# Optimization experiments

Measured on AMD Instinct MI355X. Metric: run time of the kernel, lower is better.

## Reference

```python
import jax, jax.numpy as jnp
import numpy as np

B, N, K = 2, 1280, 48
C_NODE, C_EDGE, C_OUT = 384, 128, 128
C_BIAS = C_NODE // 2          # 192 (node_dilation=2)
HID = 2 * C_BIAS + C_EDGE     # 512
LN_EPS = 1e-5


def setup_inputs() -> dict:
    key = jax.random.key(0)
    ks = jax.random.split(key, 13)
    w = lambda k, shape: (jax.random.normal(k, shape, jnp.float32) * 0.02)
    return {
        "node_emb": jax.random.normal(ks[0], (B, N, C_NODE), jnp.float32),
        "edge_emb": jax.random.normal(ks[1], (B, N, K, C_EDGE), jnp.float32),
        "E_idx": jax.random.randint(ks[2], (B, N, K), 0, N),
        "Wi": w(ks[3], (C_NODE, C_BIAS)), "bi": jnp.zeros((C_BIAS,), jnp.float32),
        "W1": w(ks[4], (HID, HID)), "b1": jnp.zeros((HID,), jnp.float32),
        "W2": w(ks[5], (HID, HID)), "b2": jnp.zeros((HID,), jnp.float32),
        "Wf": w(ks[6], (HID, C_OUT)), "bf": jnp.zeros((C_OUT,), jnp.float32),
        "gamma": jnp.ones((C_OUT,), jnp.float32),
        "beta": jnp.zeros((C_OUT,), jnp.float32),
    }


def reference(node_emb, edge_emb, E_idx, Wi, bi, W1, b1, W2, b2, Wf, bf, gamma, beta):
    # initial_embed: [B, N, C_NODE] -> [B, N, C_BIAS]
    n = node_emb @ Wi + bi
    # edge_bias[b,i,k] = concat(n[b,i], n[b, E_idx[b,i,k]])  (tile + gather_edges fused)
    nbr = jax.vmap(lambda v, e: v[e])(n, E_idx)                     # [B, N, K, C_BIAS]
    slf = jnp.broadcast_to(n[:, :, None, :], nbr.shape)             # [B, N, K, C_BIAS]
    x = jnp.concatenate([edge_emb, slf, nbr], axis=-1)              # [B, N, K, HID]
    h = jax.nn.relu(x @ W1 + b1)
    h = jax.nn.relu(h @ W2 + b2)
    # final_layer on residual sum, then LayerNorm
    y = (h + x) @ Wf + bf                                           # [B, N, K, C_OUT]
    mu = jnp.mean(y, axis=-1, keepdims=True)
    var = jnp.mean((y - mu) ** 2, axis=-1, keepdims=True)
    return (y - mu) * jax.lax.rsqrt(var + LN_EPS) * gamma + beta
```

## Files before the change

kernel.cpp:

```cpp
#include <hip/hip_runtime.h>
#include <stdint.h>

#define BB    2
#define NN    1280
#define KK    48
#define CN    384
#define CE    128
#define CB    192
#define HID   512
#define CO    128
#define MM    (BB*NN*KK)
#define CH    (MM/2)

typedef __bf16 bf16x8 __attribute__((ext_vector_type(8)));
typedef float  f32x4  __attribute__((ext_vector_type(4)));
typedef unsigned short u16x8 __attribute__((ext_vector_type(8)));

__device__ __forceinline__ unsigned short f2bf(float f) {
  unsigned int i = __builtin_bit_cast(unsigned int, f);
  unsigned int r = (i + 0x7fffu + ((i >> 16) & 1u)) >> 16;
  return (unsigned short)r;
}
__device__ __forceinline__ float bf2f(unsigned short u) {
  unsigned int v = ((unsigned int)u) << 16;
  return __builtin_bit_cast(float, v);
}

__device__ __forceinline__ void gload_lds16(const void* g, void* l) {
  __builtin_amdgcn_global_load_lds(
      (const __attribute__((address_space(1))) void*)g,
      (__attribute__((address_space(3))) void*)l, 16, 0, 0);
}

__device__ __forceinline__ void mfma_tiles(const char* ldsA, const char* ldsB,
                                           int l, int wm, int wn,
                                           f32x4 (&acc)[4][4]) {
#pragma unroll
  for (int kk = 0; kk < 2; ++kk) {
    bf16x8 av[4], bv[4];
#pragma unroll
    for (int t = 0; t < 4; ++t) {
      const int ra = wm * 64 + t * 16 + (l & 15);
      const int ca = (kk * 4 + (l >> 4)) ^ (ra & 7);
      av[t] = *(const bf16x8*)(ldsA + ra * 128 + ca * 16);
      const int rb = wn * 64 + t * 16 + (l & 15);
      const int cb = (kk * 4 + (l >> 4)) ^ (rb & 7);
      bv[t] = *(const bf16x8*)(ldsB + rb * 128 + cb * 16);
    }
#pragma unroll
    for (int mt = 0; mt < 4; ++mt)
#pragma unroll
      for (int nt = 0; nt < 4; ++nt)
        acc[mt][nt] = __builtin_amdgcn_mfma_f32_16x16x32_bf16(av[mt], bv[nt], acc[mt][nt], 0, 0, 0);
  }
}

__global__ void k_transpose_cast(const float* __restrict__ in,
                                 unsigned short* __restrict__ out,
                                 int R, int C) {
  __shared__ float tile[32][33];
  const int c0 = blockIdx.x * 32, r0 = blockIdx.y * 32;
  const int tx = threadIdx.x, ty = threadIdx.y;
#pragma unroll
  for (int dy = 0; dy < 32; dy += 8)
    tile[ty + dy][tx] = in[(size_t)(r0 + ty + dy) * C + c0 + tx];
  __syncthreads();
#pragma unroll
  for (int dy = 0; dy < 32; dy += 8)
    out[(size_t)(c0 + ty + dy) * R + r0 + tx] = f2bf(tile[tx][ty + dy]);
}

__global__ void k_node(const float* __restrict__ node,
                       const float* __restrict__ Wi,
                       const float* __restrict__ bi,
                       unsigned short* __restrict__ nbuf) {
  __shared__ float row[CN];
  const int blk = blockIdx.x;
  const float* src = node + (size_t)blk * CN;
  for (int c = threadIdx.x; c < CN; c += CB) row[c] = src[c];
  __syncthreads();
  const int t = threadIdx.x;
  float acc = bi[t];
#pragma unroll 8
  for (int c = 0; c < CN; ++c) acc += row[c] * Wi[(size_t)c * CB + t];
  nbuf[(size_t)blk * CB + t] = f2bf(acc);
}

__global__ __launch_bounds__(256, 2)
void k_gemm1(const float* __restrict__ edge,
             const unsigned short* __restrict__ nbuf,
             const int* __restrict__ eidx,
             const unsigned short* __restrict__ Wt,
             const float* __restrict__ bias,
             unsigned short* __restrict__ out,
             int mbase, int b) {
  __shared__ char lds[65536];
  const int flat = blockIdx.x;
  const int xcd = flat & 7;
  const int p = flat >> 3;
  const int m0 = (xcd * 60 + (p >> 2)) * 128;
  const int n0 = (p & 3) * 128;
  const int tid = threadIdx.x;
  const int l = tid & 63;
  const int w = tid >> 6;
  const int wm = w >> 1, wn = w & 1;
  const int sr = l >> 3, pc = l & 7;
  const int lc = pc ^ sr;

  int rr[4], big[4], nbrg[4];
  size_t mg[4];
#pragma unroll
  for (int ii = 0; ii < 4; ++ii) {
    const int r = (w * 4 + ii) * 8 + sr;
    rr[ii] = r;
    const int m = mbase + m0 + r;
    mg[ii] = (size_t)m;
    big[ii] = m / KK;
    nbrg[ii] = b * NN + eidx[m];
  }

  f32x4 acc[4][4];
#pragma unroll
  for (int i = 0; i < 4; ++i)
#pragma unroll
    for (int j = 0; j < 4; ++j) acc[i][j] = (f32x4){0.f, 0.f, 0.f, 0.f};

#pragma unroll
  for (int ii = 0; ii < 4; ++ii) {
    const int i = w * 4 + ii;
    gload_lds16(Wt + (size_t)(n0 + rr[ii]) * HID + lc * 8, lds + 16384 + i * 1024);
    const float4* ep = (const float4*)(edge + mg[ii] * CE + lc * 8);
    float4 x0 = ep[0], x1 = ep[1];
    u16x8 pk;
    pk[0] = f2bf(x0.x); pk[1] = f2bf(x0.y); pk[2] = f2bf(x0.z); pk[3] = f2bf(x0.w);
    pk[4] = f2bf(x1.x); pk[5] = f2bf(x1.y); pk[6] = f2bf(x1.z); pk[7] = f2bf(x1.w);
    *(uint4*)(lds + i * 1024 + l * 16) = __builtin_bit_cast(uint4, pk);
  }
  __syncthreads();

#pragma unroll
  for (int t = 0; t < 8; ++t) {
    char* base_c = lds + (t & 1) * 32768;
    char* base_n = lds + ((t & 1) ^ 1) * 32768;
    const int kn = (t + 1) * 64;
    float4 e0[4], e1[4];
    if (t < 7) {
#pragma unroll
      for (int ii = 0; ii < 4; ++ii) {
        const int i = w * 4 + ii;
        gload_lds16(Wt + (size_t)(n0 + rr[ii]) * HID + kn + lc * 8,
                    base_n + 16384 + i * 1024);
        if (kn < 128) {
          const float4* ep = (const float4*)(edge + mg[ii] * CE + kn + lc * 8);
          e0[ii] = ep[0];
          e1[ii] = ep[1];
        } else if (kn < 320) {
          gload_lds16(nbuf + (size_t)big[ii] * CB + (kn - 128) + lc * 8,
                      base_n + i * 1024);
        } else {
          gload_lds16(nbuf + (size_t)nbrg[ii] * CB + (kn - 320) + lc * 8,
                      base_n + i * 1024);
        }
      }
    }
    mfma_tiles(base_c, base_c + 16384, l, wm, wn, acc);
    if (t < 7 && kn < 128) {
#pragma unroll
      for (int ii = 0; ii < 4; ++ii) {
        const int i = w * 4 + ii;
        u16x8 pk;
        pk[0] = f2bf(e0[ii].x); pk[1] = f2bf(e0[ii].y);
        pk[2] = f2bf(e0[ii].z); pk[3] = f2bf(e0[ii].w);
        pk[4] = f2bf(e1[ii].x); pk[5] = f2bf(e1[ii].y);
        pk[6] = f2bf(e1[ii].z); pk[7] = f2bf(e1[ii].w);
        *(uint4*)(base_n + i * 1024 + l * 16) = __builtin_bit_cast(uint4, pk);
      }
    }
    __syncthreads();
  }

  unsigned short* tile = (unsigned short*)lds;
  const int q = l >> 4, cc = l & 15;
#pragma unroll
  for (int nt = 0; nt < 4; ++nt) {
    const int col = wn * 64 + nt * 16 + cc;
    const float bvv = bias[n0 + col];
    const int cn = col >> 3, cb = col & 7;
#pragma unroll
    for (int mt = 0; mt < 4; ++mt) {
      const int r0_ = wm * 64 + mt * 16 + q * 4;
#pragma unroll
      for (int r = 0; r < 4; ++r) {
        float v = acc[mt][nt][r] + bvv;
        v = v > 0.f ? v : 0.f;
        const int row = r0_ + r;
        tile[row * 128 + ((cn ^ (row & 7)) << 3) + cb] = f2bf(v);
      }
    }
  }
  __syncthreads();
#pragma unroll
  for (int i = 0; i < 8; ++i) {
    const int c = i * 256 + tid;
    const int row = c >> 4, cn = c & 15;
    u16x8 vv = *(const u16x8*)(tile + row * 128 + ((cn ^ (row & 7)) << 3));
    *(u16x8*)(out + (size_t)(m0 + row) * HID + n0 + cn * 8) = vv;
  }
}

__global__ __launch_bounds__(256, 2)
void k_gemm2(const unsigned short* __restrict__ A,
             const unsigned short* __restrict__ Wt,
             const float* __restrict__ bias,
             const float* __restrict__ edge,
             const unsigned short* __restrict__ nbuf,
             const int* __restrict__ eidx,
             unsigned short* __restrict__ out,
             int mbase, int b) {
  __shared__ char lds[65536];
  const int flat = blockIdx.x;
  const int xcd = flat & 7;
  const int p = flat >> 3;
  const int m0 = (xcd * 60 + (p >> 2)) * 128;
  const int n0 = (p & 3) * 128;
  const int tid = threadIdx.x;
  const int l = tid & 63;
  const int w = tid >> 6;
  const int wm = w >> 1, wn = w & 1;
  const int sr = l >> 3, pc = l & 7;
  const int lc = pc ^ sr;

  f32x4 acc[4][4];
#pragma unroll
  for (int i = 0; i < 4; ++i)
#pragma unroll
    for (int j = 0; j < 4; ++j) acc[i][j] = (f32x4){0.f, 0.f, 0.f, 0.f};

#pragma unroll
  for (int ii = 0; ii < 4; ++ii) {
    const int i = w * 4 + ii;
    const int r = i * 8 + sr;
    gload_lds16(A  + (size_t)(m0 + r) * HID + lc * 8, lds + i * 1024);
    gload_lds16(Wt + (size_t)(n0 + r) * HID + lc * 8, lds + 16384 + i * 1024);
  }
  __syncthreads();

#pragma unroll
  for (int t = 0; t < 8; ++t) {
    char* base_c = lds + (t & 1) * 32768;
    char* base_n = lds + ((t & 1) ^ 1) * 32768;
    const int kn = (t + 1) * 64;
    if (t < 7) {
#pragma unroll
      for (int ii = 0; ii < 4; ++ii) {
        const int i = w * 4 + ii;
        const int r = i * 8 + sr;
        gload_lds16(A  + (size_t)(m0 + r) * HID + kn + lc * 8, base_n + i * 1024);
        gload_lds16(Wt + (size_t)(n0 + r) * HID + kn + lc * 8, base_n + 16384 + i * 1024);
      }
    }
    mfma_tiles(base_c, base_c + 16384, l, wm, wn, acc);
    __syncthreads();
  }

  unsigned short* tile = (unsigned short*)lds;
  const int q = l >> 4, cc = l & 15;
#pragma unroll
  for (int nt = 0; nt < 4; ++nt) {
    const int col = wn * 64 + nt * 16 + cc;
    const float bvv = bias[n0 + col];
    const int cn = col >> 3, cb = col & 7;
#pragma unroll
    for (int mt = 0; mt < 4; ++mt) {
      const int r0_ = wm * 64 + mt * 16 + q * 4;
#pragma unroll
      for (int r = 0; r < 4; ++r) {
        float v = acc[mt][nt][r] + bvv;
        v = v > 0.f ? v : 0.f;
        const int row = r0_ + r;
        tile[row * 128 + ((cn ^ (row & 7)) << 3) + cb] = f2bf(v);
      }
    }
  }
  __syncthreads();
#pragma unroll
  for (int i = 0; i < 8; ++i) {
    const int c = i * 256 + tid;
    const int row = c >> 4, cn = c & 15;
    u16x8 vv = *(const u16x8*)(tile + row * 128 + ((cn ^ (row & 7)) << 3));
    const int m = mbase + m0 + row;
    float rv[8];
    if (n0 == 0) {
      const float4* ep = (const float4*)(edge + (size_t)m * CE + cn * 8);
      float4 x0 = ep[0], x1 = ep[1];
      rv[0] = x0.x; rv[1] = x0.y; rv[2] = x0.z; rv[3] = x0.w;
      rv[4] = x1.x; rv[5] = x1.y; rv[6] = x1.z; rv[7] = x1.w;
    } else if (n0 == 128) {
      u16x8 xv = *(const u16x8*)(nbuf + (size_t)(m / KK) * CB + cn * 8);
#pragma unroll
      for (int j = 0; j < 8; ++j) rv[j] = bf2f(xv[j]);
    } else if (n0 == 256) {
      u16x8 xv;
      if (cn < 8) {
        xv = *(const u16x8*)(nbuf + (size_t)(m / KK) * CB + 128 + cn * 8);
      } else {
        const int e = eidx[m];
        xv = *(const u16x8*)(nbuf + (size_t)(b * NN + e) * CB + cn * 8 - 64);
      }
#pragma unroll
      for (int j = 0; j < 8; ++j) rv[j] = bf2f(xv[j]);
    } else {
      const int e = eidx[m];
      u16x8 xv = *(const u16x8*)(nbuf + (size_t)(b * NN + e) * CB + 64 + cn * 8);
#pragma unroll
      for (int j = 0; j < 8; ++j) rv[j] = bf2f(xv[j]);
    }
#pragma unroll
    for (int j = 0; j < 8; ++j) vv[j] = f2bf(bf2f(vv[j]) + rv[j]);
    *(u16x8*)(out + (size_t)(m0 + row) * HID + n0 + cn * 8) = vv;
  }
}

__global__ __launch_bounds__(256, 2)
void k_final(const unsigned short* __restrict__ A,
             const unsigned short* __restrict__ Wft,
             const float* __restrict__ bias,
             const float* __restrict__ gamma,
             const float* __restrict__ beta,
             float* __restrict__ out) {
  __shared__ char lds[65536];
  const int m0 = blockIdx.x * 128;
  const int tid = threadIdx.x;
  const int l = tid & 63;
  const int w = tid >> 6;
  const int sr = l >> 3, pc = l & 7;
  const int lc = pc ^ sr;

  f32x4 acc[2][8];
#pragma unroll
  for (int i = 0; i < 2; ++i)
#pragma unroll
    for (int j = 0; j < 8; ++j) acc[i][j] = (f32x4){0.f, 0.f, 0.f, 0.f};

#pragma unroll
  for (int ii = 0; ii < 4; ++ii) {
    const int i = w * 4 + ii;
    const int r = i * 8 + sr;
    gload_lds16(A   + (size_t)(m0 + r) * HID + lc * 8, lds + i * 1024);
    gload_lds16(Wft + (size_t)r * HID + lc * 8,        lds + 16384 + i * 1024);
  }
  __syncthreads();

#pragma unroll
  for (int t = 0; t < 8; ++t) {
    char* ldsA = lds + (t & 1) * 32768;
    char* ldsB = ldsA + 16384;
    char* base_n = lds + ((t & 1) ^ 1) * 32768;
    const int kn = (t + 1) * 64;
    if (t < 7) {
#pragma unroll
      for (int ii = 0; ii < 4; ++ii) {
        const int i = w * 4 + ii;
        const int r = i * 8 + sr;
        gload_lds16(A   + (size_t)(m0 + r) * HID + kn + lc * 8, base_n + i * 1024);
        gload_lds16(Wft + (size_t)r * HID + kn + lc * 8,        base_n + 16384 + i * 1024);
      }
    }
#pragma unroll
    for (int kk = 0; kk < 2; ++kk) {
      bf16x8 av[2], bv[8];
#pragma unroll
      for (int tt = 0; tt < 2; ++tt) {
        const int ra = w * 32 + tt * 16 + (l & 15);
        const int ca = (kk * 4 + (l >> 4)) ^ (ra & 7);
        av[tt] = *(const bf16x8*)(ldsA + ra * 128 + ca * 16);
      }
#pragma unroll
      for (int tt = 0; tt < 8; ++tt) {
        const int rb = tt * 16 + (l & 15);
        const int cb = (kk * 4 + (l >> 4)) ^ (rb & 7);
        bv[tt] = *(const bf16x8*)(ldsB + rb * 128 + cb * 16);
      }
#pragma unroll
      for (int mt = 0; mt < 2; ++mt)
#pragma unroll
        for (int nt = 0; nt < 8; ++nt)
          acc[mt][nt] = __builtin_amdgcn_mfma_f32_16x16x32_bf16(av[mt], bv[nt], acc[mt][nt], 0, 0, 0);
    }
    __syncthreads();
  }

  const int q = l >> 4, cc = l & 15;
  float gg[8], bb[8], bs[8];
#pragma unroll
  for (int j = 0; j < 8; ++j) {
    const int col = j * 16 + cc;
    gg[j] = gamma[col];
    bb[j] = beta[col];
    bs[j] = bias[col];
  }
#pragma unroll
  for (int mt = 0; mt < 2; ++mt) {
#pragma unroll
    for (int r = 0; r < 4; ++r) {
      float s = 0.f, ss = 0.f;
#pragma unroll
      for (int j = 0; j < 8; ++j) {
        const float v = acc[mt][j][r] + bs[j];
        acc[mt][j][r] = v;
        s += v;
        ss += v * v;
      }
#pragma unroll
      for (int mk = 1; mk < 16; mk <<= 1) {
        s  += __shfl_xor(s, mk, 64);
        ss += __shfl_xor(ss, mk, 64);
      }
      const float mu = s * (1.f / 128.f);
      const float var = ss * (1.f / 128.f) - mu * mu;
      const float rstd = rsqrtf(var + 1e-5f);
      const int row = m0 + w * 32 + mt * 16 + q * 4 + r;
#pragma unroll
      for (int j = 0; j < 8; ++j) {
        const float v = (acc[mt][j][r] - mu) * rstd * gg[j] + bb[j];
        out[(size_t)row * CO + j * 16 + cc] = v;
      }
    }
  }
}

#define O_N    ((size_t)0)
#define O_WT1  ((size_t)0x100000)
#define O_WT2  (O_WT1 + (size_t)0x80000)
#define O_WFT  (O_WT2 + (size_t)0x80000)
#define O_H1   ((size_t)0x300000)
#define O_A    (O_H1 + (size_t)CH * HID * 2)

extern "C" void kernel_launch(void* const* d_in, const int* in_sizes, int n_in,
                              void* d_out, int out_size, void* d_ws, size_t ws_size,
                              hipStream_t stream) {
  const float* node  = (const float*)d_in[0];
  const float* edge  = (const float*)d_in[1];
  const int*   eidx  = (const int*)d_in[2];
  const float* Wi    = (const float*)d_in[3];
  const float* bi    = (const float*)d_in[4];
  const float* W1    = (const float*)d_in[5];
  const float* b1    = (const float*)d_in[6];
  const float* W2    = (const float*)d_in[7];
  const float* b2    = (const float*)d_in[8];
  const float* Wf    = (const float*)d_in[9];
  const float* bfv   = (const float*)d_in[10];
  const float* gamma = (const float*)d_in[11];
  const float* beta  = (const float*)d_in[12];
  float* out = (float*)d_out;

  char* ws = (char*)d_ws;
  unsigned short* nbuf = (unsigned short*)(ws + O_N);
  unsigned short* Wt1  = (unsigned short*)(ws + O_WT1);
  unsigned short* Wt2  = (unsigned short*)(ws + O_WT2);
  unsigned short* Wft  = (unsigned short*)(ws + O_WFT);
  unsigned short* h1   = (unsigned short*)(ws + O_H1);
  unsigned short* abuf = (unsigned short*)(ws + O_A);

  k_transpose_cast<<<dim3(HID / 32, HID / 32), dim3(32, 8), 0, stream>>>(W1, Wt1, HID, HID);
  k_transpose_cast<<<dim3(HID / 32, HID / 32), dim3(32, 8), 0, stream>>>(W2, Wt2, HID, HID);
  k_transpose_cast<<<dim3(CO / 32, HID / 32), dim3(32, 8), 0, stream>>>(Wf, Wft, HID, CO);

  k_node<<<BB * NN, CB, 0, stream>>>(node, Wi, bi, nbuf);

  for (int c = 0; c < 2; ++c) {
    k_gemm1<<<(CH / 128) * 4, 256, 0, stream>>>(edge, nbuf, eidx, Wt1, b1, h1, c * CH, c);
    k_gemm2<<<(CH / 128) * 4, 256, 0, stream>>>(h1, Wt2, b2, edge, nbuf, eidx, abuf, c * CH, c);
    k_final<<<CH / 128, 256, 0, stream>>>(abuf, Wft, bfv, gamma, beta, out + (size_t)c * CH * CO);
  }
}
```

Baseline: 422.2 us.

## Replace syncthreads with explicit vmcnt waits and barriers in GEMM pipelines

Swaps the full __syncthreads (which drains all outstanding memory ops) for explicit s_waitcnt vmcnt(N) counts plus s_barrier, so prefetches of the next K-slice can stay in flight while the current slice is consumed. It also raises wave priority around the MFMA block, and restructures the first kernel's edge-embedding prologue to issue loads before conversion. This relies on hand-counted vmcnt values matching the number of outstanding loads, which is fragile and can cause races if the compiler reorders or merges loads.

Measured after the change: 406.2 us. 1.04x faster.

```diff
diff --git a/kernel.cpp b/kernel.cpp
--- a/kernel.cpp
+++ b/kernel.cpp
@@ -15,6 +15,11 @@
 typedef __bf16 bf16x8 __attribute__((ext_vector_type(8)));
 typedef float  f32x4  __attribute__((ext_vector_type(4)));
 typedef unsigned short u16x8 __attribute__((ext_vector_type(8)));
+
+#define VMCNT(n)  asm volatile("s_waitcnt vmcnt(" #n ")" ::: "memory")
+#define LGKM0()   asm volatile("s_waitcnt lgkmcnt(0)" ::: "memory")
+#define MEMFENCE() asm volatile("" ::: "memory")
+#define BAR()     __builtin_amdgcn_s_barrier()
 
 __device__ __forceinline__ unsigned short f2bf(float f) {
   unsigned int i = __builtin_bit_cast(unsigned int, f);
@@ -125,59 +130,88 @@
 #pragma unroll
     for (int j = 0; j < 4; ++j) acc[i][j] = (f32x4){0.f, 0.f, 0.f, 0.f};
 
-#pragma unroll
-  for (int ii = 0; ii < 4; ++ii) {
-    const int i = w * 4 + ii;
-    gload_lds16(Wt + (size_t)(n0 + rr[ii]) * HID + lc * 8, lds + 16384 + i * 1024);
-    const float4* ep = (const float4*)(edge + mg[ii] * CE + lc * 8);
-    float4 x0 = ep[0], x1 = ep[1];
-    u16x8 pk;
-    pk[0] = f2bf(x0.x); pk[1] = f2bf(x0.y); pk[2] = f2bf(x0.z); pk[3] = f2bf(x0.w);
-    pk[4] = f2bf(x1.x); pk[5] = f2bf(x1.y); pk[6] = f2bf(x1.z); pk[7] = f2bf(x1.w);
-    *(uint4*)(lds + i * 1024 + l * 16) = __builtin_bit_cast(uint4, pk);
-  }
-  __syncthreads();
+  {
+    float4 p0[4], p1[4];
+#pragma unroll
+    for (int ii = 0; ii < 4; ++ii) {
+      const float4* ep = (const float4*)(edge + mg[ii] * CE + lc * 8);
+      p0[ii] = ep[0];
+      p1[ii] = ep[1];
+    }
+#pragma unroll
+    for (int ii = 0; ii < 4; ++ii)
+      gload_lds16(Wt + (size_t)(n0 + rr[ii]) * HID + lc * 8,
+                  lds + 16384 + (w * 4 + ii) * 1024);
+#pragma unroll
+    for (int ii = 0; ii < 4; ++ii) {
+      u16x8 pk;
+      pk[0] = f2bf(p0[ii].x); pk[1] = f2bf(p0[ii].y);
+      pk[2] = f2bf(p0[ii].z); pk[3] = f2bf(p0[ii].w);
+      pk[4] = f2bf(p1[ii].x); pk[5] = f2bf(p1[ii].y);
+      pk[6] = f2bf(p1[ii].z); pk[7] = f2bf(p1[ii].w);
+      *(uint4*)(lds + (w * 4 + ii) * 1024 + l * 16) = __builtin_bit_cast(uint4, pk);
+    }
+  }
 
 #pragma unroll
   for (int t = 0; t < 8; ++t) {
-    char* base_c = lds + (t & 1) * 32768;
+    const char* base_c = lds + (t & 1) * 32768;
     char* base_n = lds + ((t & 1) ^ 1) * 32768;
     const int kn = (t + 1) * 64;
     float4 e0[4], e1[4];
-    if (t < 7) {
+    if (t == 0) {
+#pragma unroll
+      for (int ii = 0; ii < 4; ++ii) {
+        const float4* ep = (const float4*)(edge + mg[ii] * CE + 64 + lc * 8);
+        e0[ii] = ep[0];
+        e1[ii] = ep[1];
+      }
+#pragma unroll
+      for (int ii = 0; ii < 4; ++ii)
+        gload_lds16(Wt + (size_t)(n0 + rr[ii]) * HID + 64 + lc * 8,
+                    base_n + 16384 + (w * 4 + ii) * 1024);
+      VMCNT(12);
+      LGKM0();
+    } else if (t < 7) {
 #pragma unroll
       for (int ii = 0; ii < 4; ++ii) {
         const int i = w * 4 + ii;
+        if (kn < 320)
+          gload_lds16(nbuf + (size_t)big[ii] * CB + (kn - 128) + lc * 8,
+                      base_n + i * 1024);
+        else
+          gload_lds16(nbuf + (size_t)nbrg[ii] * CB + (kn - 320) + lc * 8,
+                      base_n + i * 1024);
         gload_lds16(Wt + (size_t)(n0 + rr[ii]) * HID + kn + lc * 8,
                     base_n + 16384 + i * 1024);
-        if (kn < 128) {
-          const float4* ep = (const float4*)(edge + mg[ii] * CE + kn + lc * 8);
-          e0[ii] = ep[0];
-          e1[ii] = ep[1];
-        } else if (kn < 320) {
-          gload_lds16(nbuf + (size_t)big[ii] * CB + (kn - 128) + lc * 8,
-                      base_n + i * 1024);
-        } else {
-          gload_lds16(nbuf + (size_t)nbrg[ii] * CB + (kn - 320) + lc * 8,
-                      base_n + i * 1024);
-        }
-      }
-    }
+      }
+      VMCNT(8);
+    } else {
+      VMCNT(0);
+    }
+    BAR();
+    MEMFENCE();
+    __builtin_amdgcn_s_setprio(1);
     mfma_tiles(base_c, base_c + 16384, l, wm, wn, acc);
-    if (t < 7 && kn < 128) {
+    __builtin_amdgcn_s_setprio(0);
+    if (t == 0) {
 #pragma unroll
       for (int ii = 0; ii < 4; ++ii) {
-        const int i = w * 4 + ii;
         u16x8 pk;
         pk[0] = f2bf(e0[ii].x); pk[1] = f2bf(e0[ii].y);
         pk[2] = f2bf(e0[ii].z); pk[3] = f2bf(e0[ii].w);
         pk[4] = f2bf(e1[ii].x); pk[5] = f2bf(e1[ii].y);
         pk[6] = f2bf(e1[ii].z); pk[7] = f2bf(e1[ii].w);
-        *(uint4*)(base_n + i * 1024 + l * 16) = __builtin_bit_cast(uint4, pk);
-      }
-    }
-    __syncthreads();
-  }
+        *(uint4*)(base_n + (w * 4 + ii) * 1024 + l * 16) = __builtin_bit_cast(uint4, pk);
+      }
+      LGKM0();
+      BAR();
+    } else if (t < 7) {
+      MEMFENCE();
+      BAR();
+    }
+  }
+  __syncthreads();
 
   unsigned short* tile = (unsigned short*)lds;
   const int q = l >> 4, cc = l & 15;
@@ -243,11 +277,10 @@
     gload_lds16(A  + (size_t)(m0 + r) * HID + lc * 8, lds + i * 1024);
     gload_lds16(Wt + (size_t)(n0 + r) * HID + lc * 8, lds + 16384 + i * 1024);
   }
-  __syncthreads();
 
 #pragma unroll
   for (int t = 0; t < 8; ++t) {
-    char* base_c = lds + (t & 1) * 32768;
+    const char* base_c = lds + (t & 1) * 32768;
     char* base_n = lds + ((t & 1) ^ 1) * 32768;
     const int kn = (t + 1) * 64;
     if (t < 7) {
@@ -258,10 +291,21 @@
         gload_lds16(A  + (size_t)(m0 + r) * HID + kn + lc * 8, base_n + i * 1024);
         gload_lds16(Wt + (size_t)(n0 + r) * HID + kn + lc * 8, base_n + 16384 + i * 1024);
       }
-    }
+      VMCNT(8);
+    } else {
+      VMCNT(0);
+    }
+    BAR();
+    MEMFENCE();
+    __builtin_amdgcn_s_setprio(1);
     mfma_tiles(base_c, base_c + 16384, l, wm, wn, acc);
-    __syncthreads();
-  }
+    __builtin_amdgcn_s_setprio(0);
+    if (t < 7) {
+      MEMFENCE();
+      BAR();
+    }
+  }
+  __syncthreads();
 
   unsigned short* tile = (unsigned short*)lds;
   const int q = l >> 4, cc = l & 15;
@@ -349,12 +393,11 @@
     gload_lds16(A   + (size_t)(m0 + r) * HID + lc * 8, lds + i * 1024);
     gload_lds16(Wft + (size_t)r * HID + lc * 8,        lds + 16384 + i * 1024);
   }
-  __syncthreads();
 
 #pragma unroll
   for (int t = 0; t < 8; ++t) {
-    char* ldsA = lds + (t & 1) * 32768;
-    char* ldsB = ldsA + 16384;
+    const char* ldsA = lds + (t & 1) * 32768;
+    const char* ldsB = ldsA + 16384;
     char* base_n = lds + ((t & 1) ^ 1) * 32768;
     const int kn = (t + 1) * 64;
     if (t < 7) {
@@ -365,7 +408,13 @@
         gload_lds16(A   + (size_t)(m0 + r) * HID + kn + lc * 8, base_n + i * 1024);
         gload_lds16(Wft + (size_t)r * HID + kn + lc * 8,        base_n + 16384 + i * 1024);
       }
-    }
+      VMCNT(8);
+    } else {
+      VMCNT(0);
+    }
+    BAR();
+    MEMFENCE();
+    __builtin_amdgcn_s_setprio(1);
 #pragma unroll
     for (int kk = 0; kk < 2; ++kk) {
       bf16x8 av[2], bv[8];
@@ -387,7 +436,11 @@
         for (int nt = 0; nt < 8; ++nt)
           acc[mt][nt] = __builtin_amdgcn_mfma_f32_16x16x32_bf16(av[mt], bv[nt], acc[mt][nt], 0, 0, 0);
     }
-    __syncthreads();
+    __builtin_amdgcn_s_setprio(0);
+    if (t < 7) {
+      MEMFENCE();
+      BAR();
+    }
   }
 
   const int q = l >> 4, cc = l & 15;
```
